# Kernel tuning notes

Hardware: AMD Instinct MI355X
Metric: run time of the kernel (lower is better)

## Reference

```python
import jax, jax.numpy as jnp
import numpy as np

N, E, H, C = 50000, 800000, 4, 64
IN_DIM = 128
HID = H * C            # 256, concat output width
VH = C // 2            # 32, value-head hidden
OUT_DIM = 4
NEG_SLOPE = 0.2
LN_EPS = 1e-5


def setup_inputs() -> dict:
    key = jax.random.key(0)
    ks = iter(jax.random.split(key, 64))
    def nrm(shape, s=0.05):
        return jax.random.normal(next(ks), shape, jnp.float32) * s
    inp = {
        "x": jax.random.normal(next(ks), (N, IN_DIM), jnp.float32),
        "edge_src": jax.random.randint(next(ks), (E,), 0, N, dtype=jnp.int32),
        "edge_dst": jax.random.randint(next(ks), (E,), 0, N, dtype=jnp.int32),
        "proj_w": nrm((C, IN_DIM)),
        "proj_b": jnp.zeros((C,), jnp.float32),
    }
    in_dims = [C, HID, HID]
    out_feats = [HID, HID, C]
    for i in range(3):
        inp[f"w{i}"] = nrm((HID, in_dims[i]))
        inp[f"asrc{i}"] = nrm((H, C))
        inp[f"adst{i}"] = nrm((H, C))
        inp[f"b{i}"] = jnp.zeros((out_feats[i],), jnp.float32)
        inp[f"g{i}"] = jnp.ones((out_feats[i],), jnp.float32)
        inp[f"be{i}"] = jnp.zeros((out_feats[i],), jnp.float32)
    inp["vw1"] = nrm((VH, C)); inp["vb1"] = jnp.zeros((VH,), jnp.float32)
    inp["vw2"] = nrm((OUT_DIM, VH)); inp["vb2"] = jnp.zeros((OUT_DIM,), jnp.float32)
    return inp


def _layer_norm(x, g, b):
    mu = x.mean(-1, keepdims=True)
    var = ((x - mu) ** 2).mean(-1, keepdims=True)
    return (x - mu) * jax.lax.rsqrt(var + LN_EPS) * g + b


def _gat_conv(x, src, dst, w, a_s, a_d, bias, concat):
    # x: [N, in_dim] -> h: [N, H, C]
    n = x.shape[0]
    h = (x @ w.T).reshape(n, H, C)
    asrc = jnp.einsum('nhc,hc->nh', h, a_s)  # [N, H]
    adst = jnp.einsum('nhc,hc->nh', h, a_d)
    # PyG default add_self_loops=True
    loop = jnp.arange(n, dtype=src.dtype)
    src_f = jnp.concatenate([src, loop])
    dst_f = jnp.concatenate([dst, loop])
    alpha = jax.nn.leaky_relu(asrc[src_f] + adst[dst_f], NEG_SLOPE)  # [E+N, H]
    # segment softmax over incoming edges of each destination node
    amax = jax.ops.segment_max(alpha, dst_f, num_segments=n)
    ex = jnp.exp(alpha - amax[dst_f])
    denom = jax.ops.segment_sum(ex, dst_f, num_segments=n)
    coef = ex / (denom[dst_f] + 1e-16)
    out = jax.ops.segment_sum(h[src_f] * coef[:, :, None], dst_f, num_segments=n)
    out = out.reshape(n, H * C) if concat else out.mean(axis=1)
    return out + bias


def _gat_layer(x, src, dst, w, a_s, a_d, bias, g, be, concat):
    # GATConv -> LayerNorm -> ELU (dropout is identity in eval)
    return jax.nn.elu(_layer_norm(_gat_conv(x, src, dst, w, a_s, a_d, bias, concat), g, be))


def reference(x, edge_src, edge_dst, proj_w, proj_b,
              w0, asrc0, adst0, b0, g0, be0,
              w1, asrc1, adst1, b1, g1, be1,
              w2, asrc2, adst2, b2, g2, be2,
              vw1, vb1, vw2, vb2):
    h = jax.nn.elu(x @ proj_w.T + proj_b)
    h = _gat_layer(h, edge_src, edge_dst, w0, asrc0, adst0, b0, g0, be0, True)
    h = _gat_layer(h, edge_src, edge_dst, w1, asrc1, adst1, b1, g1, be1, True)
    h = _gat_layer(h, edge_src, edge_dst, w2, asrc2, adst2, b2, g2, be2, False)
    v = jax.nn.elu(h @ vw1.T + vb1)
    return v @ vw2.T + vb2
```

## Files before the change

### kernel.cpp

```cpp
#include <hip/hip_runtime.h>

typedef unsigned short u16;
typedef u16 u16x4 __attribute__((ext_vector_type(4)));
typedef short short8 __attribute__((ext_vector_type(8)));
typedef float f32x4 __attribute__((ext_vector_type(4)));

__device__ __forceinline__ float elu_f(float x) { return x > 0.f ? x : expm1f(x); }
__device__ __forceinline__ float lrelu_f(float x) { return x > 0.f ? x : 0.2f * x; }

__device__ __forceinline__ u16 f2b(float f) {
  union { float f; unsigned u; } v; v.f = f;
  unsigned r = v.u + 0x7FFF + ((v.u >> 16) & 1);
  return (u16)(r >> 16);
}
__device__ __forceinline__ float b2f(u16 u) {
  union { unsigned u; float f; } v; v.u = ((unsigned)u) << 16; return v.f;
}

__global__ __launch_bounds__(256) void cvtdeg_k(const float* __restrict__ x, u16* __restrict__ xb,
                                                int nx8,
                                                const float* __restrict__ pw,
                                                const float* __restrict__ w0,
                                                const float* __restrict__ w1,
                                                const float* __restrict__ w2,
                                                u16* __restrict__ dp, u16* __restrict__ d0,
                                                u16* __restrict__ d1, u16* __restrict__ d2,
                                                const int* __restrict__ edst,
                                                int E, int n, int* __restrict__ deg) {
  int i = blockIdx.x * 256 + threadIdx.x;
  if (i < nx8) {
    int j = i * 8;
    float4 a = *reinterpret_cast<const float4*>(&x[j]);
    float4 b = *reinterpret_cast<const float4*>(&x[j + 4]);
    u16x4 o0, o1;
    o0.x = f2b(a.x); o0.y = f2b(a.y); o0.z = f2b(a.z); o0.w = f2b(a.w);
    o1.x = f2b(b.x); o1.y = f2b(b.y); o1.z = f2b(b.z); o1.w = f2b(b.w);
    *reinterpret_cast<u16x4*>(&xb[j]) = o0;
    *reinterpret_cast<u16x4*>(&xb[j + 4]) = o1;
  } else if (i < nx8 + 155648) {
    int j = i - nx8;
    if (j < 8192) dp[j] = f2b(pw[j]);
    else if (j < 24576) d0[j - 8192] = f2b(w0[j - 8192]);
    else if (j < 90112) d1[j - 24576] = f2b(w1[j - 24576]);
    else d2[j - 90112] = f2b(w2[j - 90112]);
  } else {
    int j = i - (nx8 + 155648);
    if (j < E) atomicAdd(&deg[edst[j]], 1);
    else if (j < E + n) atomicAdd(&deg[j - E], 1);
  }
}

__global__ __launch_bounds__(256) void block_sum_k(const int* __restrict__ deg,
                                                   int* __restrict__ bsum, int n) {
  int i = blockIdx.x * 256 + threadIdx.x;
  int v = (i < n) ? deg[i] : 0;
#pragma unroll
  for (int off = 1; off < 64; off <<= 1) v += __shfl_xor(v, off);
  __shared__ int ws[4];
  if ((threadIdx.x & 63) == 0) ws[threadIdx.x >> 6] = v;
  __syncthreads();
  if (threadIdx.x == 0) bsum[blockIdx.x] = ws[0] + ws[1] + ws[2] + ws[3];
}

__global__ void scan_bsum_k(int* __restrict__ bsum, int nb) {
  __shared__ int s[1024];
  int tid = threadIdx.x;
  int v = (tid < nb) ? bsum[tid] : 0;
  s[tid] = v;
  __syncthreads();
  for (int off = 1; off < 1024; off <<= 1) {
    int t = (tid >= off) ? s[tid - off] : 0;
    __syncthreads();
    s[tid] += t;
    __syncthreads();
  }
  if (tid < nb) bsum[tid] = s[tid] - v;
}

__global__ __launch_bounds__(256) void block_scan_k(const int* __restrict__ deg,
                                                    const int* __restrict__ bsum,
                                                    int* __restrict__ rowptr,
                                                    int* __restrict__ cursor, int n) {
  int i = blockIdx.x * 256 + threadIdx.x;
  int lane = threadIdx.x & 63, w = threadIdx.x >> 6;
  int v = (i < n) ? deg[i] : 0;
  int x = v;
#pragma unroll
  for (int off = 1; off < 64; off <<= 1) {
    int t = __shfl_up(x, off);
    if (lane >= off) x += t;
  }
  __shared__ int ws[4];
  if (lane == 63) ws[w] = x;
  __syncthreads();
  int add = bsum[blockIdx.x];
  for (int j = 0; j < w; ++j) add += ws[j];
  int excl = x - v + add;
  if (i < n) {
    cursor[i] = excl;
    rowptr[i + 1] = excl + v;
  }
  if (i == 0) rowptr[0] = 0;
}

__global__ void scatter_k(const int* __restrict__ src, const int* __restrict__ dst,
                          int E, int n, int* __restrict__ cursor,
                          int* __restrict__ col, int* __restrict__ dst2) {
  int e = blockIdx.x * blockDim.x + threadIdx.x;
  if (e < E) {
    int d = dst[e];
    int pos = atomicAdd(&cursor[d], 1);
    col[pos] = src[e];
    dst2[pos] = d;
  } else if (e < E + n) {
    int d = e - E;
    int pos = atomicAdd(&cursor[d], 1);
    col[pos] = d;
    dst2[pos] = d;
  }
}

template <int PROJ>
__global__ __launch_bounds__(512) void gemm2_k(const u16* __restrict__ A, int lda,
                                               const u16* __restrict__ W,
                                               const u16* __restrict__ pw,
                                               const float* __restrict__ pb,
                                               u16* __restrict__ Cb,
                                               int n, int K,
                                               const float* __restrict__ a_sv,
                                               const float* __restrict__ a_dv,
                                               float* __restrict__ asrcN,
                                               float* __restrict__ adstN) {
  __shared__ char Asb[128 * 128];
  __shared__ char Bsb[256 * 128];
  __shared__ char Xsb[PROJ ? 128 * 272 : 16];
  __shared__ char Psb[PROJ ? 64 * 272 : 16];
  const int t = threadIdx.x;
  const int lane = t & 63, w = t >> 6;
  const int wrow = w >> 2, wcol = w & 3;
  const int row0 = blockIdx.x * 128;

  if (PROJ) {
#pragma unroll
    for (int i = 0; i < 4; ++i) {
      int ci = i * 512 + t;
      int r = ci >> 4;
      int b = (ci & 15) << 4;
      int ar = row0 + r; ar = ar < n ? ar : n - 1;
      *reinterpret_cast<int4*>(Xsb + r * 272 + b) =
          *reinterpret_cast<const int4*>(&A[(size_t)ar * 128 + (b >> 1)]);
    }
#pragma unroll
    for (int i = 0; i < 2; ++i) {
      int ci = i * 512 + t;
      int r = ci >> 4;
      int b = (ci & 15) << 4;
      *reinterpret_cast<int4*>(Psb + r * 272 + b) =
          *reinterpret_cast<const int4*>(&pw[r * 128 + (b >> 1)]);
    }
    __syncthreads();
    f32x4 pacc[4];
#pragma unroll
    for (int nf = 0; nf < 4; ++nf) pacc[nf] = (f32x4){0.f, 0.f, 0.f, 0.f};
#pragma unroll
    for (int ks = 0; ks < 4; ++ks) {
      short8 paf = *reinterpret_cast<const short8*>(
          Xsb + (w * 16 + (lane & 15)) * 272 + ks * 64 + (lane >> 4) * 16);
#pragma unroll
      for (int nf = 0; nf < 4; ++nf) {
        short8 pbf = *reinterpret_cast<const short8*>(
            Psb + (nf * 16 + (lane & 15)) * 272 + ks * 64 + (lane >> 4) * 16);
        pacc[nf] = __builtin_amdgcn_mfma_f32_16x16x32_bf16(paf, pbf, pacc[nf], 0, 0, 0);
      }
    }
#pragma unroll
    for (int nf = 0; nf < 4; ++nf) {
#pragma unroll
      for (int j = 0; j < 4; ++j) {
        int rl = w * 16 + (lane >> 4) * 4 + j;
        int cg = nf * 16 + (lane & 15);
        u16 bv = f2b(elu_f(pacc[nf][j] + pb[cg]));
        *reinterpret_cast<u16*>(Asb + rl * 128 + ((cg * 2) ^ ((rl & 7) << 4))) = bv;
      }
    }
  }

  f32x4 acc[4][4];
#pragma unroll
  for (int m = 0; m < 4; ++m)
#pragma unroll
    for (int nf = 0; nf < 4; ++nf) acc[m][nf] = (f32x4){0.f, 0.f, 0.f, 0.f};

  for (int k0 = 0; k0 < K; k0 += 64) {
    if (!PROJ) {
#pragma unroll
      for (int i = 0; i < 2; ++i) {
        int ci = i * 512 + t;
        int r = ci >> 3;
        int b = (ci & 7) << 4;
        int sw = b ^ ((r & 7) << 4);
        int ar = row0 + r; ar = ar < n ? ar : n - 1;
        int4 av = *reinterpret_cast<const int4*>(&A[(size_t)ar * lda + k0 + (b >> 1)]);
        *reinterpret_cast<int4*>(Asb + r * 128 + sw) = av;
      }
    }
#pragma unroll
    for (int i = 0; i < 4; ++i) {
      int ci = i * 512 + t;
      int r = ci >> 3;
      int b = (ci & 7) << 4;
      int sw = b ^ ((r & 7) << 4);
      int4 wv = *reinterpret_cast<const int4*>(&W[(size_t)r * K + k0 + (b >> 1)]);
      *reinterpret_cast<int4*>(Bsb + r * 128 + sw) = wv;
    }
    __syncthreads();
#pragma unroll
    for (int ks = 0; ks < 2; ++ks) {
      short8 af[4], bf[4];
      int kb = ks * 64 + ((lane >> 4) << 4);
#pragma unroll
      for (int m = 0; m < 4; ++m) {
        int r = wrow * 64 + m * 16 + (lane & 15);
        af[m] = *reinterpret_cast<const short8*>(Asb + r * 128 + (kb ^ ((r & 7) << 4)));
      }
#pragma unroll
      for (int nf = 0; nf < 4; ++nf) {
        int r = wcol * 64 + nf * 16 + (lane & 15);
        bf[nf] = *reinterpret_cast<const short8*>(Bsb + r * 128 + (kb ^ ((r & 7) << 4)));
      }
#pragma unroll
      for (int m = 0; m < 4; ++m)
#pragma unroll
        for (int nf = 0; nf < 4; ++nf)
          acc[m][nf] = __builtin_amdgcn_mfma_f32_16x16x32_bf16(af[m], bf[nf], acc[m][nf], 0, 0, 0);
    }
    __syncthreads();
  }
#pragma unroll
  for (int m = 0; m < 4; ++m) {
#pragma unroll
    for (int j = 0; j < 4; ++j) {
      int rg = row0 + wrow * 64 + m * 16 + (lane >> 4) * 4 + j;
      if (rg >= n) continue;
#pragma unroll
      for (int nf = 0; nf < 4; ++nf) {
        int cg = wcol * 64 + nf * 16 + (lane & 15);
        Cb[(size_t)rg * 256 + cg] = f2b(acc[m][nf][j]);
      }
    }
  }
  {
    int h = wcol;
    int ch = lane & 15;
    float as_c[4], ad_c[4];
#pragma unroll
    for (int nf = 0; nf < 4; ++nf) {
      as_c[nf] = a_sv[h * 64 + nf * 16 + ch];
      ad_c[nf] = a_dv[h * 64 + nf * 16 + ch];
    }
#pragma unroll
    for (int m = 0; m < 4; ++m) {
#pragma unroll
      for (int j = 0; j < 4; ++j) {
        float ps = 0.f, pd = 0.f;
#pragma unroll
        for (int nf = 0; nf < 4; ++nf) {
          float v = acc[m][nf][j];
          ps += v * as_c[nf];
          pd += v * ad_c[nf];
        }
#pragma unroll
        for (int off = 1; off < 16; off <<= 1) {
          ps += __shfl_xor(ps, off);
          pd += __shfl_xor(pd, off);
        }
        int rg = row0 + wrow * 64 + m * 16 + (lane >> 4) * 4 + j;
        if ((lane & 15) == 0 && rg < n) {
          asrcN[(size_t)rg * 4 + h] = ps;
          adstN[(size_t)rg * 4 + h] = pd;
        }
      }
    }
  }
}

__global__ __launch_bounds__(256) void edge_ex2_k(const int* __restrict__ col,
                                                  const int* __restrict__ dst2,
                                                  const float* __restrict__ asrcN,
                                                  const float* __restrict__ adstN,
                                                  float* __restrict__ exT, int eep, int EE) {
  int e = blockIdx.x * 256 + threadIdx.x;
  if (e >= EE) return;
  int s = col[e], d = dst2[e];
  float4 as = *reinterpret_cast<const float4*>(&asrcN[(size_t)s * 4]);
  float4 ad = *reinterpret_cast<const float4*>(&adstN[(size_t)d * 4]);
  exT[e]            = __expf(lrelu_f(as.x + ad.x));
  exT[eep + e]      = __expf(lrelu_f(as.y + ad.y));
  exT[2 * eep + e]  = __expf(lrelu_f(as.z + ad.z));
  exT[3 * eep + e]  = __expf(lrelu_f(as.w + ad.w));
}

template <int MODE>
__global__ __launch_bounds__(256) void gat_agg4_k(const u16* __restrict__ feat,
                                                  const float* __restrict__ exT, int eep,
                                                  const int* __restrict__ rowptr,
                                                  const int* __restrict__ col,
                                                  const float* __restrict__ bias,
                                                  const float* __restrict__ g,
                                                  const float* __restrict__ be,
                                                  const float* __restrict__ vw1,
                                                  const float* __restrict__ vb1,
                                                  const float* __restrict__ vw2,
                                                  const float* __restrict__ vb2,
                                                  void* __restrict__ out, int n) {
  int wave = threadIdx.x >> 6, lane = threadIdx.x & 63;
  int node = blockIdx.x * 4 + wave;
  if (node >= n) return;
  int h = lane >> 4;
  const float* exh = exT + (size_t)h * eep;
  int s0 = rowptr[node], s1 = rowptr[node + 1];
  float ax = 0.f, ay = 0.f, az = 0.f, aw = 0.f, den = 0.f;
  int e = s0;
  for (; e + 8 <= s1; e += 8) {
    int p0 = col[e + 0], p1 = col[e + 1], p2 = col[e + 2], p3 = col[e + 3];
    int q0 = col[e + 4], q1 = col[e + 5], q2 = col[e + 6], q3 = col[e + 7];
    float u0 = exh[e + 0], u1 = exh[e + 1], u2 = exh[e + 2], u3 = exh[e + 3];
    float v0 = exh[e + 4], v1 = exh[e + 5], v2 = exh[e + 6], v3 = exh[e + 7];
    u16x4 fp0 = *reinterpret_cast<const u16x4*>(&feat[(size_t)p0 * 256 + lane * 4]);
    u16x4 fp1 = *reinterpret_cast<const u16x4*>(&feat[(size_t)p1 * 256 + lane * 4]);
    u16x4 fp2 = *reinterpret_cast<const u16x4*>(&feat[(size_t)p2 * 256 + lane * 4]);
    u16x4 fp3 = *reinterpret_cast<const u16x4*>(&feat[(size_t)p3 * 256 + lane * 4]);
    u16x4 fq0 = *reinterpret_cast<const u16x4*>(&feat[(size_t)q0 * 256 + lane * 4]);
    u16x4 fq1 = *reinterpret_cast<const u16x4*>(&feat[(size_t)q1 * 256 + lane * 4]);
    u16x4 fq2 = *reinterpret_cast<const u16x4*>(&feat[(size_t)q2 * 256 + lane * 4]);
    u16x4 fq3 = *reinterpret_cast<const u16x4*>(&feat[(size_t)q3 * 256 + lane * 4]);
    den += ((u0 + u1) + (u2 + u3)) + ((v0 + v1) + (v2 + v3));
    ax += u0 * b2f(fp0.x) + u1 * b2f(fp1.x) + u2 * b2f(fp2.x) + u3 * b2f(fp3.x);
    ay += u0 * b2f(fp0.y) + u1 * b2f(fp1.y) + u2 * b2f(fp2.y) + u3 * b2f(fp3.y);
    az += u0 * b2f(fp0.z) + u1 * b2f(fp1.z) + u2 * b2f(fp2.z) + u3 * b2f(fp3.z);
    aw += u0 * b2f(fp0.w) + u1 * b2f(fp1.w) + u2 * b2f(fp2.w) + u3 * b2f(fp3.w);
    ax += v0 * b2f(fq0.x) + v1 * b2f(fq1.x) + v2 * b2f(fq2.x) + v3 * b2f(fq3.x);
    ay += v0 * b2f(fq0.y) + v1 * b2f(fq1.y) + v2 * b2f(fq2.y) + v3 * b2f(fq3.y);
    az += v0 * b2f(fq0.z) + v1 * b2f(fq1.z) + v2 * b2f(fq2.z) + v3 * b2f(fq3.z);
    aw += v0 * b2f(fq0.w) + v1 * b2f(fq1.w) + v2 * b2f(fq2.w) + v3 * b2f(fq3.w);
  }
  for (; e + 4 <= s1; e += 4) {
    int p0 = col[e + 0], p1 = col[e + 1], p2 = col[e + 2], p3 = col[e + 3];
    float u0 = exh[e + 0], u1 = exh[e + 1], u2 = exh[e + 2], u3 = exh[e + 3];
    u16x4 fp0 = *reinterpret_cast<const u16x4*>(&feat[(size_t)p0 * 256 + lane * 4]);
    u16x4 fp1 = *reinterpret_cast<const u16x4*>(&feat[(size_t)p1 * 256 + lane * 4]);
    u16x4 fp2 = *reinterpret_cast<const u16x4*>(&feat[(size_t)p2 * 256 + lane * 4]);
    u16x4 fp3 = *reinterpret_cast<const u16x4*>(&feat[(size_t)p3 * 256 + lane * 4]);
    den += (u0 + u1) + (u2 + u3);
    ax += u0 * b2f(fp0.x) + u1 * b2f(fp1.x) + u2 * b2f(fp2.x) + u3 * b2f(fp3.x);
    ay += u0 * b2f(fp0.y) + u1 * b2f(fp1.y) + u2 * b2f(fp2.y) + u3 * b2f(fp3.y);
    az += u0 * b2f(fp0.z) + u1 * b2f(fp1.z) + u2 * b2f(fp2.z) + u3 * b2f(fp3.z);
    aw += u0 * b2f(fp0.w) + u1 * b2f(fp1.w) + u2 * b2f(fp2.w) + u3 * b2f(fp3.w);
  }
  for (; e < s1; ++e) {
    int s = col[e];
    float xv = exh[e];
    den += xv;
    u16x4 f = *reinterpret_cast<const u16x4*>(&feat[(size_t)s * 256 + lane * 4]);
    ax += xv * b2f(f.x); ay += xv * b2f(f.y); az += xv * b2f(f.z); aw += xv * b2f(f.w);
  }
  float inv = 1.f / den;
  ax *= inv; ay *= inv; az *= inv; aw *= inv;

  if (MODE == 0) {
    float4 b4 = *reinterpret_cast<const float4*>(&bias[lane * 4]);
    float vx = ax + b4.x, vy = ay + b4.y, vz = az + b4.z, vw = aw + b4.w;
    float s = vx + vy + vz + vw;
#pragma unroll
    for (int off = 1; off < 64; off <<= 1) s += __shfl_xor(s, off);
    float mu = s * (1.f / 256.f);
    float dx = vx - mu, dy = vy - mu, dz = vz - mu, dw = vw - mu;
    float q = dx * dx + dy * dy + dz * dz + dw * dw;
#pragma unroll
    for (int off = 1; off < 64; off <<= 1) q += __shfl_xor(q, off);
    float inv2 = rsqrtf(q * (1.f / 256.f) + 1e-5f);
    float4 gg = *reinterpret_cast<const float4*>(&g[lane * 4]);
    float4 bb = *reinterpret_cast<const float4*>(&be[lane * 4]);
    u16x4 o;
    o.x = f2b(elu_f(dx * inv2 * gg.x + bb.x));
    o.y = f2b(elu_f(dy * inv2 * gg.y + bb.y));
    o.z = f2b(elu_f(dz * inv2 * gg.z + bb.z));
    o.w = f2b(elu_f(dw * inv2 * gg.w + bb.w));
    u16* rowb = (u16*)out + (size_t)node * 256;
    *reinterpret_cast<u16x4*>(&rowb[lane * 4]) = o;
  } else {
    ax += __shfl_xor(ax, 16); ax += __shfl_xor(ax, 32);
    ay += __shfl_xor(ay, 16); ay += __shfl_xor(ay, 32);
    az += __shfl_xor(az, 16); az += __shfl_xor(az, 32);
    aw += __shfl_xor(aw, 16); aw += __shfl_xor(aw, 32);
    int qd = lane & 15;
    float4 b4 = *reinterpret_cast<const float4*>(&bias[qd * 4]);
    float vx = 0.25f * ax + b4.x, vy = 0.25f * ay + b4.y;
    float vz = 0.25f * az + b4.z, vw = 0.25f * aw + b4.w;
    float s = vx + vy + vz + vw;
#pragma unroll
    for (int off = 1; off < 64; off <<= 1) s += __shfl_xor(s, off);
    float mu = s * (1.f / 256.f);
    float dx = vx - mu, dy = vy - mu, dz = vz - mu, dw = vw - mu;
    float q = dx * dx + dy * dy + dz * dz + dw * dw;
#pragma unroll
    for (int off = 1; off < 64; off <<= 1) q += __shfl_xor(q, off);
    float inv2 = rsqrtf(q * (1.f / 256.f) + 1e-5f);
    float4 gg = *reinterpret_cast<const float4*>(&g[qd * 4]);
    float4 bb = *reinterpret_cast<const float4*>(&be[qd * 4]);
    float h0 = elu_f(dx * inv2 * gg.x + bb.x);
    float h1 = elu_f(dy * inv2 * gg.y + bb.y);
    float h2 = elu_f(dz * inv2 * gg.z + bb.z);
    float h3 = elu_f(dw * inv2 * gg.w + bb.w);
    int r = (lane >> 4) & 3;
    float pj[8];
#pragma unroll
    for (int jj = 0; jj < 8; ++jj) {
      int j = r * 8 + jj;
      float4 wv = *reinterpret_cast<const float4*>(&vw1[(size_t)j * 64 + qd * 4]);
      pj[jj] = h0 * wv.x + h1 * wv.y + h2 * wv.z + h3 * wv.w;
    }
#pragma unroll
    for (int off = 1; off < 16; off <<= 1) {
#pragma unroll
      for (int jj = 0; jj < 8; ++jj) pj[jj] += __shfl_xor(pj[jj], off);
    }
    float4 vb1a = *reinterpret_cast<const float4*>(&vb1[r * 8]);
    float4 vb1b = *reinterpret_cast<const float4*>(&vb1[r * 8 + 4]);
    float vj0 = elu_f(pj[0] + vb1a.x), vj1 = elu_f(pj[1] + vb1a.y);
    float vj2 = elu_f(pj[2] + vb1a.z), vj3 = elu_f(pj[3] + vb1a.w);
    float vj4 = elu_f(pj[4] + vb1b.x), vj5 = elu_f(pj[5] + vb1b.y);
    float vj6 = elu_f(pj[6] + vb1b.z), vj7 = elu_f(pj[7] + vb1b.w);
    float qo[4];
#pragma unroll
    for (int o = 0; o < 4; ++o) {
      float4 w2a = *reinterpret_cast<const float4*>(&vw2[o * 32 + r * 8]);
      float4 w2b = *reinterpret_cast<const float4*>(&vw2[o * 32 + r * 8 + 4]);
      qo[o] = vj0 * w2a.x + vj1 * w2a.y + vj2 * w2a.z + vj3 * w2a.w +
              vj4 * w2b.x + vj5 * w2b.y + vj6 * w2b.z + vj7 * w2b.w;
    }
#pragma unroll
    for (int o = 0; o < 4; ++o) {
      qo[o] += __shfl_xor(qo[o], 16);
      qo[o] += __shfl_xor(qo[o], 32);
    }
    if (lane == 0) {
      float4 vb2v = *reinterpret_cast<const float4*>(&vb2[0]);
      float4 o4;
      o4.x = qo[0] + vb2v.x; o4.y = qo[1] + vb2v.y;
      o4.z = qo[2] + vb2v.z; o4.w = qo[3] + vb2v.w;
      *reinterpret_cast<float4*>(&((float*)out)[(size_t)node * 4]) = o4;
    }
  }
}

extern "C" void kernel_launch(void* const* d_in, const int* in_sizes, int n_in,
                              void* d_out, int out_size, void* d_ws, size_t ws_size,
                              hipStream_t stream) {
  const float* x      = (const float*)d_in[0];
  const int*   esrc   = (const int*)d_in[1];
  const int*   edst   = (const int*)d_in[2];
  const float* proj_w = (const float*)d_in[3];
  const float* proj_b = (const float*)d_in[4];
  const float* w[3]   = {(const float*)d_in[5],  (const float*)d_in[11], (const float*)d_in[17]};
  const float* a_s[3] = {(const float*)d_in[6],  (const float*)d_in[12], (const float*)d_in[18]};
  const float* a_d[3] = {(const float*)d_in[7],  (const float*)d_in[13], (const float*)d_in[19]};
  const float* bb[3]  = {(const float*)d_in[8],  (const float*)d_in[14], (const float*)d_in[20]};
  const float* gg[3]  = {(const float*)d_in[9],  (const float*)d_in[15], (const float*)d_in[21]};
  const float* be[3]  = {(const float*)d_in[10], (const float*)d_in[16], (const float*)d_in[22]};
  const float* vw1 = (const float*)d_in[23];
  const float* vb1 = (const float*)d_in[24];
  const float* vw2 = (const float*)d_in[25];
  const float* vb2 = (const float*)d_in[26];
  float* outp = (float*)d_out;

  const int n = in_sizes[0] / 128;
  const int E = in_sizes[1];
  const int EE = E + n;
  const int eep = (EE + 255) & ~255;
  const int nbl = (n + 255) / 256;

  char* p = (char*)d_ws;
  auto alloc = [&](size_t bytes) { char* r = p; p += (bytes + 255) & ~(size_t)255; return r; };
  u16*   hA    = (u16*)alloc((size_t)n * 512);
  u16*   featB = (u16*)alloc((size_t)n * 512);
  u16*   xb    = (u16*)alloc((size_t)n * 256);
  float* exT   = (float*)alloc((size_t)eep * 16);
  float* asrcN = (float*)alloc((size_t)n * 16);
  float* adstN = (float*)alloc((size_t)n * 16);
  u16* wbp = (u16*)alloc(64 * 128 * 2);
  u16* wb[3];
  wb[0] = (u16*)alloc(256 * 64 * 2);
  wb[1] = (u16*)alloc(256 * 256 * 2);
  wb[2] = (u16*)alloc(256 * 256 * 2);
  int* deg    = (int*)alloc((size_t)n * 4);
  int* rowptr = (int*)alloc((size_t)(n + 1) * 4);
  int* cursor = (int*)alloc((size_t)n * 4);
  int* col    = (int*)alloc((size_t)EE * 4);
  int* dst2   = (int*)alloc((size_t)EE * 4);
  int* bsum   = (int*)alloc((size_t)nbl * 4);

  hipMemsetAsync(deg, 0, (size_t)n * sizeof(int), stream);
  const int nx8 = n * 16;
  cvtdeg_k<<<(nx8 + 155648 + EE + 255) / 256, 256, 0, stream>>>(
      x, xb, nx8, proj_w, w[0], w[1], w[2], wbp, wb[0], wb[1], wb[2], edst, E, n, deg);
  block_sum_k<<<nbl, 256, 0, stream>>>(deg, bsum, n);
  scan_bsum_k<<<1, 1024, 0, stream>>>(bsum, nbl);
  block_scan_k<<<nbl, 256, 0, stream>>>(deg, bsum, rowptr, cursor, n);
  scatter_k<<<(EE + 255) / 256, 256, 0, stream>>>(esrc, edst, E, n, cursor, col, dst2);

  const int nb4 = (n + 3) / 4;
  const int nbg = (n + 127) / 128;
  dim3 blk(256);

  const int Kin[3] = {64, 256, 256};
  for (int i = 0; i < 3; ++i) {
    if (i == 0) {
      gemm2_k<1><<<nbg, 512, 0, stream>>>(xb, 128, wb[0], wbp, proj_b, featB,
                                          n, 64, a_s[0], a_d[0], asrcN, adstN);
    } else {
      gemm2_k<0><<<nbg, 512, 0, stream>>>(hA, 256, wb[i], nullptr, nullptr, featB,
                                          n, Kin[i], a_s[i], a_d[i], asrcN, adstN);
    }
    edge_ex2_k<<<(EE + 255) / 256, 256, 0, stream>>>(col, dst2, asrcN, adstN, exT, eep, EE);
    if (i < 2) {
      gat_agg4_k<0><<<nb4, blk, 0, stream>>>(featB, exT, eep, rowptr, col, bb[i], gg[i], be[i],
                                             nullptr, nullptr, nullptr, nullptr, (void*)hA, n);
    } else {
      gat_agg4_k<1><<<nb4, blk, 0, stream>>>(featB, exT, eep, rowptr, col, bb[i], gg[i], be[i],
                                             vw1, vb1, vw2, vb2, (void*)outp, n);
    }
  }
}
```

Measured before the change: 400.0 us.

## Use grid-stride persistent waves for GAT aggregation and split value head into own kernel

The aggregation kernel now launches at most 2048 blocks and each wave loops over nodes with a grid stride instead of one wave per node. The final-layer MLP value head is moved out of the aggregation kernel into a separate kernel that stages vw1 in shared memory. The aggregation kernel writes fp32 hidden features to a buffer for the head to read. This is meant to cut block launch overhead and register pressure in the aggregation kernel, at the cost of an extra launch and an extra global round-trip of N×64 floats.

```diff
diff --git a/kernel.cpp b/kernel.cpp
--- a/kernel.cpp
+++ b/kernel.cpp
@@ -301,156 +301,150 @@
 }
 
 template <int MODE>
-__global__ __launch_bounds__(256) void gat_agg4_k(const u16* __restrict__ feat,
+__global__ __launch_bounds__(256) void gat_agg5_k(const u16* __restrict__ feat,
                                                   const float* __restrict__ exT, int eep,
                                                   const int* __restrict__ rowptr,
                                                   const int* __restrict__ col,
                                                   const float* __restrict__ bias,
                                                   const float* __restrict__ g,
                                                   const float* __restrict__ be,
-                                                  const float* __restrict__ vw1,
-                                                  const float* __restrict__ vb1,
-                                                  const float* __restrict__ vw2,
-                                                  const float* __restrict__ vb2,
-                                                  void* __restrict__ out, int n) {
+                                                  void* __restrict__ out, int n, int nwaves) {
   int wave = threadIdx.x >> 6, lane = threadIdx.x & 63;
-  int node = blockIdx.x * 4 + wave;
-  if (node >= n) return;
+  int wid = blockIdx.x * 4 + wave;
   int h = lane >> 4;
   const float* exh = exT + (size_t)h * eep;
-  int s0 = rowptr[node], s1 = rowptr[node + 1];
-  float ax = 0.f, ay = 0.f, az = 0.f, aw = 0.f, den = 0.f;
-  int e = s0;
-  for (; e + 8 <= s1; e += 8) {
-    int p0 = col[e + 0], p1 = col[e + 1], p2 = col[e + 2], p3 = col[e + 3];
-    int q0 = col[e + 4], q1 = col[e + 5], q2 = col[e + 6], q3 = col[e + 7];
-    float u0 = exh[e + 0], u1 = exh[e + 1], u2 = exh[e + 2], u3 = exh[e + 3];
-    float v0 = exh[e + 4], v1 = exh[e + 5], v2 = exh[e + 6], v3 = exh[e + 7];
-    u16x4 fp0 = *reinterpret_cast<const u16x4*>(&feat[(size_t)p0 * 256 + lane * 4]);
-    u16x4 fp1 = *reinterpret_cast<const u16x4*>(&feat[(size_t)p1 * 256 + lane * 4]);
-    u16x4 fp2 = *reinterpret_cast<const u16x4*>(&feat[(size_t)p2 * 256 + lane * 4]);
-    u16x4 fp3 = *reinterpret_cast<const u16x4*>(&feat[(size_t)p3 * 256 + lane * 4]);
-    u16x4 fq0 = *reinterpret_cast<const u16x4*>(&feat[(size_t)q0 * 256 + lane * 4]);
-    u16x4 fq1 = *reinterpret_cast<const u16x4*>(&feat[(size_t)q1 * 256 + lane * 4]);
-    u16x4 fq2 = *reinterpret_cast<const u16x4*>(&feat[(size_t)q2 * 256 + lane * 4]);
-    u16x4 fq3 = *reinterpret_cast<const u16x4*>(&feat[(size_t)q3 * 256 + lane * 4]);
-    den += ((u0 + u1) + (u2 + u3)) + ((v0 + v1) + (v2 + v3));
-    ax += u0 * b2f(fp0.x) + u1 * b2f(fp1.x) + u2 * b2f(fp2.x) + u3 * b2f(fp3.x);
-    ay += u0 * b2f(fp0.y) + u1 * b2f(fp1.y) + u2 * b2f(fp2.y) + u3 * b2f(fp3.y);
-    az += u0 * b2f(fp0.z) + u1 * b2f(fp1.z) + u2 * b2f(fp2.z) + u3 * b2f(fp3.z);
-    aw += u0 * b2f(fp0.w) + u1 * b2f(fp1.w) + u2 * b2f(fp2.w) + u3 * b2f(fp3.w);
-    ax += v0 * b2f(fq0.x) + v1 * b2f(fq1.x) + v2 * b2f(fq2.x) + v3 * b2f(fq3.x);
-    ay += v0 * b2f(fq0.y) + v1 * b2f(fq1.y) + v2 * b2f(fq2.y) + v3 * b2f(fq3.y);
-    az += v0 * b2f(fq0.z) + v1 * b2f(fq1.z) + v2 * b2f(fq2.z) + v3 * b2f(fq3.z);
-    aw += v0 * b2f(fq0.w) + v1 * b2f(fq1.w) + v2 * b2f(fq2.w) + v3 * b2f(fq3.w);
-  }
-  for (; e + 4 <= s1; e += 4) {
-    int p0 = col[e + 0], p1 = col[e + 1], p2 = col[e + 2], p3 = col[e + 3];
-    float u0 = exh[e + 0], u1 = exh[e + 1], u2 = exh[e + 2], u3 = exh[e + 3];
-    u16x4 fp0 = *reinterpret_cast<const u16x4*>(&feat[(size_t)p0 * 256 + lane * 4]);
-    u16x4 fp1 = *reinterpret_cast<const u16x4*>(&feat[(size_t)p1 * 256 + lane * 4]);
-    u16x4 fp2 = *reinterpret_cast<const u16x4*>(&feat[(size_t)p2 * 256 + lane * 4]);
-    u16x4 fp3 = *reinterpret_cast<const u16x4*>(&feat[(size_t)p3 * 256 + lane * 4]);
-    den += (u0 + u1) + (u2 + u3);
-    ax += u0 * b2f(fp0.x) + u1 * b2f(fp1.x) + u2 * b2f(fp2.x) + u3 * b2f(fp3.x);
-    ay += u0 * b2f(fp0.y) + u1 * b2f(fp1.y) + u2 * b2f(fp2.y) + u3 * b2f(fp3.y);
-    az += u0 * b2f(fp0.z) + u1 * b2f(fp1.z) + u2 * b2f(fp2.z) + u3 * b2f(fp3.z);
-    aw += u0 * b2f(fp0.w) + u1 * b2f(fp1.w) + u2 * b2f(fp2.w) + u3 * b2f(fp3.w);
-  }
-  for (; e < s1; ++e) {
-    int s = col[e];
-    float xv = exh[e];
-    den += xv;
-    u16x4 f = *reinterpret_cast<const u16x4*>(&feat[(size_t)s * 256 + lane * 4]);
-    ax += xv * b2f(f.x); ay += xv * b2f(f.y); az += xv * b2f(f.z); aw += xv * b2f(f.w);
-  }
-  float inv = 1.f / den;
-  ax *= inv; ay *= inv; az *= inv; aw *= inv;
-
-  if (MODE == 0) {
-    float4 b4 = *reinterpret_cast<const float4*>(&bias[lane * 4]);
-    float vx = ax + b4.x, vy = ay + b4.y, vz = az + b4.z, vw = aw + b4.w;
-    float s = vx + vy + vz + vw;
-#pragma unroll
-    for (int off = 1; off < 64; off <<= 1) s += __shfl_xor(s, off);
-    float mu = s * (1.f / 256.f);
-    float dx = vx - mu, dy = vy - mu, dz = vz - mu, dw = vw - mu;
-    float q = dx * dx + dy * dy + dz * dz + dw * dw;
-#pragma unroll
-    for (int off = 1; off < 64; off <<= 1) q += __shfl_xor(q, off);
-    float inv2 = rsqrtf(q * (1.f / 256.f) + 1e-5f);
-    float4 gg = *reinterpret_cast<const float4*>(&g[lane * 4]);
-    float4 bb = *reinterpret_cast<const float4*>(&be[lane * 4]);
-    u16x4 o;
-    o.x = f2b(elu_f(dx * inv2 * gg.x + bb.x));
-    o.y = f2b(elu_f(dy * inv2 * gg.y + bb.y));
-    o.z = f2b(elu_f(dz * inv2 * gg.z + bb.z));
-    o.w = f2b(elu_f(dw * inv2 * gg.w + bb.w));
-    u16* rowb = (u16*)out + (size_t)node * 256;
-    *reinterpret_cast<u16x4*>(&rowb[lane * 4]) = o;
-  } else {
-    ax += __shfl_xor(ax, 16); ax += __shfl_xor(ax, 32);
-    ay += __shfl_xor(ay, 16); ay += __shfl_xor(ay, 32);
-    az += __shfl_xor(az, 16); az += __shfl_xor(az, 32);
-    aw += __shfl_xor(aw, 16); aw += __shfl_xor(aw, 32);
-    int qd = lane & 15;
-    float4 b4 = *reinterpret_cast<const float4*>(&bias[qd * 4]);
-    float vx = 0.25f * ax + b4.x, vy = 0.25f * ay + b4.y;
-    float vz = 0.25f * az + b4.z, vw = 0.25f * aw + b4.w;
-    float s = vx + vy + vz + vw;
-#pragma unroll
-    for (int off = 1; off < 64; off <<= 1) s += __shfl_xor(s, off);
-    float mu = s * (1.f / 256.f);
-    float dx = vx - mu, dy = vy - mu, dz = vz - mu, dw = vw - mu;
-    float q = dx * dx + dy * dy + dz * dz + dw * dw;
-#pragma unroll
-    for (int off = 1; off < 64; off <<= 1) q += __shfl_xor(q, off);
-    float inv2 = rsqrtf(q * (1.f / 256.f) + 1e-5f);
-    float4 gg = *reinterpret_cast<const float4*>(&g[qd * 4]);
-    float4 bb = *reinterpret_cast<const float4*>(&be[qd * 4]);
-    float h0 = elu_f(dx * inv2 * gg.x + bb.x);
-    float h1 = elu_f(dy * inv2 * gg.y + bb.y);
-    float h2 = elu_f(dz * inv2 * gg.z + bb.z);
-    float h3 = elu_f(dw * inv2 * gg.w + bb.w);
-    int r = (lane >> 4) & 3;
-    float pj[8];
-#pragma unroll
-    for (int jj = 0; jj < 8; ++jj) {
-      int j = r * 8 + jj;
-      float4 wv = *reinterpret_cast<const float4*>(&vw1[(size_t)j * 64 + qd * 4]);
-      pj[jj] = h0 * wv.x + h1 * wv.y + h2 * wv.z + h3 * wv.w;
-    }
-#pragma unroll
-    for (int off = 1; off < 16; off <<= 1) {
-#pragma unroll
-      for (int jj = 0; jj < 8; ++jj) pj[jj] += __shfl_xor(pj[jj], off);
-    }
-    float4 vb1a = *reinterpret_cast<const float4*>(&vb1[r * 8]);
-    float4 vb1b = *reinterpret_cast<const float4*>(&vb1[r * 8 + 4]);
-    float vj0 = elu_f(pj[0] + vb1a.x), vj1 = elu_f(pj[1] + vb1a.y);
-    float vj2 = elu_f(pj[2] + vb1a.z), vj3 = elu_f(pj[3] + vb1a.w);
-    float vj4 = elu_f(pj[4] + vb1b.x), vj5 = elu_f(pj[5] + vb1b.y);
-    float vj6 = elu_f(pj[6] + vb1b.z), vj7 = elu_f(pj[7] + vb1b.w);
-    float qo[4];
-#pragma unroll
-    for (int o = 0; o < 4; ++o) {
-      float4 w2a = *reinterpret_cast<const float4*>(&vw2[o * 32 + r * 8]);
-      float4 w2b = *reinterpret_cast<const float4*>(&vw2[o * 32 + r * 8 + 4]);
-      qo[o] = vj0 * w2a.x + vj1 * w2a.y + vj2 * w2a.z + vj3 * w2a.w +
-              vj4 * w2b.x + vj5 * w2b.y + vj6 * w2b.z + vj7 * w2b.w;
-    }
-#pragma unroll
-    for (int o = 0; o < 4; ++o) {
-      qo[o] += __shfl_xor(qo[o], 16);
-      qo[o] += __shfl_xor(qo[o], 32);
-    }
-    if (lane == 0) {
-      float4 vb2v = *reinterpret_cast<const float4*>(&vb2[0]);
-      float4 o4;
-      o4.x = qo[0] + vb2v.x; o4.y = qo[1] + vb2v.y;
-      o4.z = qo[2] + vb2v.z; o4.w = qo[3] + vb2v.w;
-      *reinterpret_cast<float4*>(&((float*)out)[(size_t)node * 4]) = o4;
-    }
+  for (int node = wid; node < n; node += nwaves) {
+    int s0 = rowptr[node], s1 = rowptr[node + 1];
+    float ax = 0.f, ay = 0.f, az = 0.f, aw = 0.f, den = 0.f;
+    int e = s0;
+    for (; e + 8 <= s1; e += 8) {
+      int p0 = col[e + 0], p1 = col[e + 1], p2 = col[e + 2], p3 = col[e + 3];
+      int q0 = col[e + 4], q1 = col[e + 5], q2 = col[e + 6], q3 = col[e + 7];
+      float u0 = exh[e + 0], u1 = exh[e + 1], u2 = exh[e + 2], u3 = exh[e + 3];
+      float v0 = exh[e + 4], v1 = exh[e + 5], v2 = exh[e + 6], v3 = exh[e + 7];
+      u16x4 fp0 = *reinterpret_cast<const u16x4*>(&feat[(size_t)p0 * 256 + lane * 4]);
+      u16x4 fp1 = *reinterpret_cast<const u16x4*>(&feat[(size_t)p1 * 256 + lane * 4]);
+      u16x4 fp2 = *reinterpret_cast<const u16x4*>(&feat[(size_t)p2 * 256 + lane * 4]);
+      u16x4 fp3 = *reinterpret_cast<const u16x4*>(&feat[(size_t)p3 * 256 + lane * 4]);
+      u16x4 fq0 = *reinterpret_cast<const u16x4*>(&feat[(size_t)q0 * 256 + lane * 4]);
+      u16x4 fq1 = *reinterpret_cast<const u16x4*>(&feat[(size_t)q1 * 256 + lane * 4]);
+      u16x4 fq2 = *reinterpret_cast<const u16x4*>(&feat[(size_t)q2 * 256 + lane * 4]);
+      u16x4 fq3 = *reinterpret_cast<const u16x4*>(&feat[(size_t)q3 * 256 + lane * 4]);
+      den += ((u0 + u1) + (u2 + u3)) + ((v0 + v1) + (v2 + v3));
+      ax += u0 * b2f(fp0.x) + u1 * b2f(fp1.x) + u2 * b2f(fp2.x) + u3 * b2f(fp3.x);
+      ay += u0 * b2f(fp0.y) + u1 * b2f(fp1.y) + u2 * b2f(fp2.y) + u3 * b2f(fp3.y);
+      az += u0 * b2f(fp0.z) + u1 * b2f(fp1.z) + u2 * b2f(fp2.z) + u3 * b2f(fp3.z);
+      aw += u0 * b2f(fp0.w) + u1 * b2f(fp1.w) + u2 * b2f(fp2.w) + u3 * b2f(fp3.w);
+      ax += v0 * b2f(fq0.x) + v1 * b2f(fq1.x) + v2 * b2f(fq2.x) + v3 * b2f(fq3.x);
+      ay += v0 * b2f(fq0.y) + v1 * b2f(fq1.y) + v2 * b2f(fq2.y) + v3 * b2f(fq3.y);
+      az += v0 * b2f(fq0.z) + v1 * b2f(fq1.z) + v2 * b2f(fq2.z) + v3 * b2f(fq3.z);
+      aw += v0 * b2f(fq0.w) + v1 * b2f(fq1.w) + v2 * b2f(fq2.w) + v3 * b2f(fq3.w);
+    }
+    for (; e + 4 <= s1; e += 4) {
+      int p0 = col[e + 0], p1 = col[e + 1], p2 = col[e + 2], p3 = col[e + 3];
+      float u0 = exh[e + 0], u1 = exh[e + 1], u2 = exh[e + 2], u3 = exh[e + 3];
+      u16x4 fp0 = *reinterpret_cast<const u16x4*>(&feat[(size_t)p0 * 256 + lane * 4]);
+      u16x4 fp1 = *reinterpret_cast<const u16x4*>(&feat[(size_t)p1 * 256 + lane * 4]);
+      u16x4 fp2 = *reinterpret_cast<const u16x4*>(&feat[(size_t)p2 * 256 + lane * 4]);
+      u16x4 fp3 = *reinterpret_cast<const u16x4*>(&feat[(size_t)p3 * 256 + lane * 4]);
+      den += (u0 + u1) + (u2 + u3);
+      ax += u0 * b2f(fp0.x) + u1 * b2f(fp1.x) + u2 * b2f(fp2.x) + u3 * b2f(fp3.x);
+      ay += u0 * b2f(fp0.y) + u1 * b2f(fp1.y) + u2 * b2f(fp2.y) + u3 * b2f(fp3.y);
+      az += u0 * b2f(fp0.z) + u1 * b2f(fp1.z) + u2 * b2f(fp2.z) + u3 * b2f(fp3.z);
+      aw += u0 * b2f(fp0.w) + u1 * b2f(fp1.w) + u2 * b2f(fp2.w) + u3 * b2f(fp3.w);
+    }
+    for (; e < s1; ++e) {
+      int s = col[e];
+      float xv = exh[e];
+      den += xv;
+      u16x4 f = *reinterpret_cast<const u16x4*>(&feat[(size_t)s * 256 + lane * 4]);
+      ax += xv * b2f(f.x); ay += xv * b2f(f.y); az += xv * b2f(f.z); aw += xv * b2f(f.w);
+    }
+    float inv = 1.f / den;
+    ax *= inv; ay *= inv; az *= inv; aw *= inv;
+
+    if (MODE == 0) {
+      float4 b4 = *reinterpret_cast<const float4*>(&bias[lane * 4]);
+      float vx = ax + b4.x, vy = ay + b4.y, vz = az + b4.z, vw = aw + b4.w;
+      float s = vx + vy + vz + vw;
+#pragma unroll
+      for (int off = 1; off < 64; off <<= 1) s += __shfl_xor(s, off);
+      float mu = s * (1.f / 256.f);
+      float dx = vx - mu, dy = vy - mu, dz = vz - mu, dw = vw - mu;
+      float q = dx * dx + dy * dy + dz * dz + dw * dw;
+#pragma unroll
+      for (int off = 1; off < 64; off <<= 1) q += __shfl_xor(q, off);
+      float inv2 = rsqrtf(q * (1.f / 256.f) + 1e-5f);
+      float4 gg = *reinterpret_cast<const float4*>(&g[lane * 4]);
+      float4 bb = *reinterpret_cast<const float4*>(&be[lane * 4]);
+      u16x4 o;
+      o.x = f2b(elu_f(dx * inv2 * gg.x + bb.x));
+      o.y = f2b(elu_f(dy * inv2 * gg.y + bb.y));
+      o.z = f2b(elu_f(dz * inv2 * gg.z + bb.z));
+      o.w = f2b(elu_f(dw * inv2 * gg.w + bb.w));
+      u16* rowb = (u16*)out + (size_t)node * 256;
+      *reinterpret_cast<u16x4*>(&rowb[lane * 4]) = o;
+    } else {
+      ax += __shfl_xor(ax, 16); ax += __shfl_xor(ax, 32);
+      ay += __shfl_xor(ay, 16); ay += __shfl_xor(ay, 32);
+      az += __shfl_xor(az, 16); az += __shfl_xor(az, 32);
+      aw += __shfl_xor(aw, 16); aw += __shfl_xor(aw, 32);
+      int qd = lane & 15;
+      float4 b4 = *reinterpret_cast<const float4*>(&bias[qd * 4]);
+      float vx = 0.25f * ax + b4.x, vy = 0.25f * ay + b4.y;
+      float vz = 0.25f * az + b4.z, vw = 0.25f * aw + b4.w;
+      float s = vx + vy + vz + vw;
+#pragma unroll
+      for (int off = 1; off < 64; off <<= 1) s += __shfl_xor(s, off);
+      float mu = s * (1.f / 256.f);
+      float dx = vx - mu, dy = vy - mu, dz = vz - mu, dw = vw - mu;
+      float q = dx * dx + dy * dy + dz * dz + dw * dw;
+#pragma unroll
+      for (int off = 1; off < 64; off <<= 1) q += __shfl_xor(q, off);
+      float inv2 = rsqrtf(q * (1.f / 256.f) + 1e-5f);
+      if (lane < 16) {
+        float4 gg = *reinterpret_cast<const float4*>(&g[qd * 4]);
+        float4 bb = *reinterpret_cast<const float4*>(&be[qd * 4]);
+        float4 o;
+        o.x = elu_f(dx * inv2 * gg.x + bb.x);
+        o.y = elu_f(dy * inv2 * gg.y + bb.y);
+        o.z = elu_f(dz * inv2 * gg.z + bb.z);
+        o.w = elu_f(dw * inv2 * gg.w + bb.w);
+        *reinterpret_cast<float4*>(&((float*)out)[(size_t)node * 64 + qd * 4]) = o;
+      }
+    }
+  }
+}
+
+__global__ __launch_bounds__(256) void value_head_k(const float* __restrict__ hh,
+                                                    const float* __restrict__ vw1,
+                                                    const float* __restrict__ vb1,
+                                                    const float* __restrict__ vw2,
+                                                    const float* __restrict__ vb2,
+                                                    float* __restrict__ out, int n) {
+  __shared__ float w1s[32 * 65];
+  __shared__ float hs[4][64];
+  __shared__ float vs[4][33];
+  int tid = threadIdx.x;
+  for (int i = tid; i < 2048; i += 256) w1s[(i >> 6) * 65 + (i & 63)] = vw1[i];
+  int wave = tid >> 6, lane = tid & 63;
+  int node = blockIdx.x * 4 + wave;
+  int nc = node < n ? node : n - 1;
+  hs[wave][lane] = hh[(size_t)nc * 64 + lane];
+  __syncthreads();
+  int j = lane & 31, half = lane >> 5;
+  float p = 0.f;
+#pragma unroll
+  for (int c = 0; c < 32; ++c) p += hs[wave][half * 32 + c] * w1s[j * 65 + half * 32 + c];
+  p += __shfl_xor(p, 32);
+  float v = elu_f(p + vb1[j]);
+  if (half == 0) vs[wave][j] = v;
+  __syncthreads();
+  if (lane < 4 && node < n) {
+    float o = vb2[lane];
+#pragma unroll
+    for (int jj = 0; jj < 32; ++jj) o += vs[wave][jj] * vw2[lane * 32 + jj];
+    out[(size_t)node * 4 + lane] = o;
   }
 }
 
@@ -499,6 +493,7 @@
   int* col    = (int*)alloc((size_t)EE * 4);
   int* dst2   = (int*)alloc((size_t)EE * 4);
   int* bsum   = (int*)alloc((size_t)nbl * 4);
+  float* hfinal = (float*)hA;
 
   hipMemsetAsync(deg, 0, (size_t)n * sizeof(int), stream);
   const int nx8 = n * 16;
@@ -511,6 +506,8 @@
 
   const int nb4 = (n + 3) / 4;
   const int nbg = (n + 127) / 128;
+  const int nbP = nb4 < 2048 ? nb4 : 2048;
+  const int nwaves = nbP * 4;
   dim3 blk(256);
 
   const int Kin[3] = {64, 256, 256};
@@ -524,11 +521,13 @@
     }
     edge_ex2_k<<<(EE + 255) / 256, 256, 0, stream>>>(col, dst2, asrcN, adstN, exT, eep, EE);
     if (i < 2) {
-      gat_agg4_k<0><<<nb4, blk, 0, stream>>>(featB, exT, eep, rowptr, col, bb[i], gg[i], be[i],
-                                             nullptr, nullptr, nullptr, nullptr, (void*)hA, n);
+      gat_agg5_k<0><<<nbP, blk, 0, stream>>>(featB, exT, eep, rowptr, col, bb[i], gg[i], be[i],
+                                             (void*)hA, n, nwaves);
     } else {
-      gat_agg4_k<1><<<nb4, blk, 0, stream>>>(featB, exT, eep, rowptr, col, bb[i], gg[i], be[i],
-                                             vw1, vb1, vw2, vb2, (void*)outp, n);
-    }
-  }
-}
+      gat_agg5_k<1><<<nbP, blk, 0, stream>>>(featB, exT, eep, rowptr, col, bb[i], gg[i], be[i],
+                                             (void*)hfinal, n, nwaves);
+    }
+  }
+
+  value_head_k<<<nb4, blk, 0, stream>>>(hfinal, vw1, vb1, vw2, vb2, outp, n);
+}
```

After: 438.9 us. 9.7% more time.
